# Kernel optimization log

Hardware: AMD Instinct MI355X
Metric: run time of the kernel (lower is better)

Reference implementation:

```python
import jax, jax.numpy as jnp
import numpy as np
import math

VOCAB = 32000
D_MODEL = 1024
CTX = 2048
B, T = 4, 2048
NUM_Q_HEADS = 16
NUM_KV_GROUPS = 4
HEAD_DIM = D_MODEL // NUM_Q_HEADS          # 64
REP = NUM_Q_HEADS // NUM_KV_GROUPS         # queries per KV group = 4
HALF = D_MODEL // 2                        # token/pos embedding width


def setup_inputs() -> dict:
    key = jax.random.key(0)
    ks = jax.random.split(key, 12)
    s = 0.02
    idx = jax.random.randint(ks[0], (B, T), 0, VOCAB, dtype=jnp.int32)
    mask = jnp.tril(jnp.ones((T, T), dtype=jnp.int32))  # causal mask, 0 = blocked
    return {
        "idx": idx,
        "mask": mask,
        "tok_table": jax.random.normal(ks[1], (VOCAB, HALF), jnp.float32) * s,
        "pos_table": jax.random.normal(ks[2], (CTX, HALF), jnp.float32) * s,
        "W_q": jax.random.normal(ks[3], (D_MODEL, D_MODEL), jnp.float32) * s,
        "b_q": jnp.zeros((D_MODEL,), jnp.float32),
        "W_k": jax.random.normal(ks[4], (D_MODEL, NUM_KV_GROUPS * HEAD_DIM), jnp.float32) * s,
        "b_k": jnp.zeros((NUM_KV_GROUPS * HEAD_DIM,), jnp.float32),
        "W_v": jax.random.normal(ks[5], (D_MODEL, NUM_KV_GROUPS * HEAD_DIM), jnp.float32) * s,
        "b_v": jnp.zeros((NUM_KV_GROUPS * HEAD_DIM,), jnp.float32),
        "W_o": jax.random.normal(ks[6], (D_MODEL, D_MODEL), jnp.float32) * s,
        "b_o": jnp.zeros((D_MODEL,), jnp.float32),
    }


def reference(idx, mask, tok_table, pos_table, W_q, b_q, W_k, b_k, W_v, b_v, W_o, b_o):
    Bd, Td = idx.shape
    # token + position embedding, concatenated along feature dim -> [B, T, D_MODEL]
    tok_emb = tok_table[idx]                              # [B, T, HALF]
    pos_emb = pos_table[jnp.arange(Td)]                   # [T, HALF]
    x = jnp.concatenate([tok_emb, jnp.broadcast_to(pos_emb, (Bd, Td, HALF))], axis=-1)

    # GQA projections
    Q = (x @ W_q + b_q).reshape(Bd, Td, NUM_Q_HEADS, HEAD_DIM).transpose(0, 2, 1, 3)   # [B,H,T,D]
    K = (x @ W_k + b_k).reshape(Bd, Td, NUM_KV_GROUPS, HEAD_DIM).transpose(0, 2, 1, 3) # [B,G,T,D]
    V = (x @ W_v + b_v).reshape(Bd, Td, NUM_KV_GROUPS, HEAD_DIM).transpose(0, 2, 1, 3)
    # repeat_interleave KV groups to match query heads (naive GQA expansion)
    K = jnp.repeat(K, REP, axis=1)                        # [B,H,T,D]
    V = jnp.repeat(V, REP, axis=1)

    scale = 1.0 / math.sqrt(HEAD_DIM)
    scores = jnp.einsum('bhqd,bhkd->bhqk', Q, K) * scale  # [B,H,T,T]
    scores = jnp.where(mask == 0, jnp.float32(-1e9), scores)
    probs = jax.nn.softmax(scores, axis=-1)
    attn = jnp.einsum('bhqk,bhkd->bhqd', probs, V)        # [B,H,T,D]
    attn = attn.transpose(0, 2, 1, 3).reshape(Bd, Td, D_MODEL)
    return attn @ W_o + b_o
```

## Files before the change

### kernel.cpp

```cpp
#include <hip/hip_runtime.h>

typedef unsigned short u16;
typedef __attribute__((ext_vector_type(8))) short bf16x8;
typedef __attribute__((ext_vector_type(4))) float f32x4;

__device__ __forceinline__ u16 f2bf(float f) {
  union { float f; unsigned u; } x; x.f = f;
  unsigned r = x.u + 0x7fffu + ((x.u >> 16) & 1u);
  return (u16)(r >> 16);
}
__device__ __forceinline__ float bf2f(u16 u) {
  union { unsigned u; float f; } x; x.u = ((unsigned)u) << 16;
  return x.f;
}

#define GLOAD_LDS16(gp, lp)                                              \
  __builtin_amdgcn_global_load_lds(                                      \
      (const __attribute__((address_space(1))) unsigned int*)(gp),       \
      (__attribute__((address_space(3))) unsigned int*)(lp), 16, 0, 0)

__global__ __launch_bounds__(256) void transpose_w(const float* __restrict__ in,
                                                   u16* __restrict__ out, int N) {
  __shared__ float tile[32][33];
  const int n0 = blockIdx.x * 32, k0 = blockIdx.y * 32;
  const int tx = threadIdx.x & 31, ty = threadIdx.x >> 5;
#pragma unroll
  for (int i = 0; i < 4; ++i) {
    int k = k0 + ty + i * 8;
    tile[ty + i * 8][tx] = in[(size_t)k * N + n0 + tx];
  }
  __syncthreads();
#pragma unroll
  for (int i = 0; i < 4; ++i) {
    int n = n0 + ty + i * 8;
    out[(size_t)n * 1024 + k0 + tx] = f2bf(tile[tx][ty + i * 8]);
  }
}

__global__ __launch_bounds__(256) void embed_kernel(const int* __restrict__ idx,
                                                    const float* __restrict__ tok,
                                                    const float* __restrict__ pos,
                                                    u16* __restrict__ x) {
  const int r = blockIdx.x;
  const int t = r & 2047;
  const int tok_id = idx[r];
  const int c = threadIdx.x * 4;
  float4 v;
  if (c < 512)
    v = *(const float4*)&tok[(size_t)tok_id * 512 + c];
  else
    v = *(const float4*)&pos[(size_t)t * 512 + (c - 512)];
  ushort4 o;
  o.x = f2bf(v.x); o.y = f2bf(v.y); o.z = f2bf(v.z); o.w = f2bf(v.w);
  *(ushort4*)&x[(size_t)r * 1024 + c] = o;
}

__global__ __launch_bounds__(256) void gemm_qkv(const u16* __restrict__ A,
                                                const u16* __restrict__ Bt,
                                                const float* __restrict__ bq,
                                                const float* __restrict__ bk,
                                                const float* __restrict__ bv,
                                                u16* __restrict__ Qb, u16* __restrict__ Kb,
                                                u16* __restrict__ Vb) {
  __shared__ u16 Alds[128 * 32];
  __shared__ u16 Blds[128 * 32];
  const int tid = threadIdx.x;
  const int lane = tid & 63, w = tid >> 6;
  const int ln = lane & 15, lm = lane >> 4;
  const int wm = w & 1, wn = w >> 1;
  const int bm = blockIdx.y, bn = blockIdx.x;
  f32x4 acc[4][4] = {};
  const size_t arow0 = (size_t)bm * 128;
  const size_t brow0 = (size_t)bn * 128;
  for (int ks = 0; ks < 1024; ks += 32) {
    __syncthreads();
#pragma unroll
    for (int it = 0; it < 2; ++it) {
      const int idx = it * 256 + tid;
      const int row = idx >> 2, ko = idx & 3;
      GLOAD_LDS16(A + (arow0 + row) * 1024 + ks + ko * 8, &Alds[idx * 8]);
      GLOAD_LDS16(Bt + (brow0 + row) * 1024 + ks + ko * 8, &Blds[idx * 8]);
    }
    asm volatile("s_waitcnt vmcnt(0)" ::: "memory");
    __syncthreads();
    bf16x8 af[4], bfr[4];
#pragma unroll
    for (int m = 0; m < 4; ++m)
      af[m] = *(const bf16x8*)&Alds[(wm * 64 + m * 16 + ln) * 32 + lm * 8];
#pragma unroll
    for (int n = 0; n < 4; ++n)
      bfr[n] = *(const bf16x8*)&Blds[(wn * 64 + n * 16 + ln) * 32 + lm * 8];
#pragma unroll
    for (int m = 0; m < 4; ++m)
#pragma unroll
      for (int n = 0; n < 4; ++n)
        acc[m][n] = __builtin_amdgcn_mfma_f32_16x16x32_bf16(af[m], bfr[n], acc[m][n], 0, 0, 0);
  }
#pragma unroll
  for (int m = 0; m < 4; ++m) {
    const int rg0 = bm * 128 + wm * 64 + m * 16 + lm * 4;
#pragma unroll
    for (int n = 0; n < 4; ++n) {
      const int cg = bn * 128 + wn * 64 + n * 16 + ln;
      float bias;
      if (cg < 1024) bias = bq[cg];
      else if (cg < 1280) bias = bk[cg - 1024];
      else bias = bv[cg - 1280];
#pragma unroll
      for (int r = 0; r < 4; ++r) {
        const int rr = rg0 + r;
        const int bb = rr >> 11, tt = rr & 2047;
        const float v = acc[m][n][r] + bias;
        if (cg < 1024) {
          Qb[(((size_t)bb * 16 + (cg >> 6)) * 2048 + tt) * 64 + (cg & 63)] = f2bf(v);
        } else if (cg < 1280) {
          const int c2 = cg - 1024;
          Kb[(((size_t)bb * 4 + (c2 >> 6)) * 2048 + tt) * 64 + (c2 & 63)] = f2bf(v);
        } else {
          const int c2 = cg - 1280;
          Vb[(((size_t)bb * 4 + (c2 >> 6)) * 2048 + tt) * 64 + (c2 & 63)] = f2bf(v);
        }
      }
    }
  }
}

__global__ __launch_bounds__(256) void transpose_v(const u16* __restrict__ V,
                                                   u16* __restrict__ Vt) {
  __shared__ u16 tile[32][33];
  const int bg = blockIdx.z;
  const int d0 = blockIdx.x * 32, t0 = blockIdx.y * 32;
  const int tx = threadIdx.x & 31, ty = threadIdx.x >> 5;
  const u16* Vin = V + (size_t)bg * 2048 * 64;
  u16* Vout = Vt + (size_t)bg * 64 * 2048;
#pragma unroll
  for (int i = 0; i < 4; ++i)
    tile[ty + i * 8][tx] = Vin[(size_t)(t0 + ty + i * 8) * 64 + d0 + tx];
  __syncthreads();
#pragma unroll
  for (int i = 0; i < 4; ++i)
    Vout[(size_t)(d0 + ty + i * 8) * 2048 + t0 + tx] = tile[tx][ty + i * 8];
}

__global__ __launch_bounds__(512) void attn_kernel(const u16* __restrict__ Qb,
                                                   const u16* __restrict__ Kb,
                                                   const u16* __restrict__ Vt,
                                                   u16* __restrict__ attn) {
  __shared__ u16 Plds[8][16 * 32];
  const int tid = threadIdx.x;
  const int lane = tid & 63, ww = tid >> 6;
  const int w = ww & 3, half = ww >> 2;
  const int ln = lane & 15, lm = lane >> 4;
  const int pair = blockIdx.x;
  const int bh = blockIdx.y;
  const int b = bh >> 4, h = bh & 15, g = h >> 2;
  const u16* Qp = Qb + (size_t)bh * 2048 * 64;
  const u16* Kp = Kb + (size_t)(b * 4 + g) * 2048 * 64;
  const u16* Vp = Vt + (size_t)(b * 4 + g) * 64 * 2048;

  const int qt = half ? (31 - pair) : pair;
  const int qw0 = qt * 64 + w * 16;

  bf16x8 qf[2];
  {
    const int qrow = qw0 + ln;
#pragma unroll
    for (int c = 0; c < 2; ++c) {
      bf16x8 raw = *(const bf16x8*)(Qp + (size_t)qrow * 64 + c * 32 + lm * 8);
#pragma unroll
      for (int i = 0; i < 8; ++i) raw[i] = (short)f2bf(bf2f((u16)raw[i]) * 0.125f);
      qf[c] = raw;
    }
  }

  f32x4 o[4] = {};
  float l_r[4] = {0.0f, 0.0f, 0.0f, 0.0f};

  const int nfull = qw0 >> 5;
  for (int kb = 0; kb <= nfull; ++kb) {
    const int kv0 = kb * 32;
    f32x4 s[2] = {};
#pragma unroll
    for (int n = 0; n < 2; ++n) {
#pragma unroll
      for (int c = 0; c < 2; ++c) {
        const bf16x8 kf =
            *(const bf16x8*)(Kp + (size_t)(kv0 + n * 16 + ln) * 64 + c * 32 + lm * 8);
        s[n] = __builtin_amdgcn_mfma_f32_16x16x32_bf16(qf[c], kf, s[n], 0, 0, 0);
      }
    }
    bf16x8 vf[4];
#pragma unroll
    for (int nd = 0; nd < 4; ++nd)
      vf[nd] = *(const bf16x8*)(Vp + (size_t)(nd * 16 + ln) * 2048 + kv0 + lm * 8);

    if (kb == nfull) {
#pragma unroll
      for (int n = 0; n < 2; ++n)
#pragma unroll
        for (int r = 0; r < 4; ++r) {
          const int kv = kv0 + n * 16 + ln;
          const int q = qw0 + lm * 4 + r;
          if (kv > q) s[n][r] = -1.0e30f;
        }
    }
#pragma unroll
    for (int n = 0; n < 2; ++n)
#pragma unroll
      for (int r = 0; r < 4; ++r) s[n][r] = __expf(s[n][r]);
#pragma unroll
    for (int r = 0; r < 4; ++r) l_r[r] += s[0][r] + s[1][r];

#pragma unroll
    for (int n = 0; n < 2; ++n)
#pragma unroll
      for (int r = 0; r < 4; ++r) {
        const int row = lm * 4 + r, col = n * 16 + ln;
        const int slot = (col >> 3) ^ ((row >> 1) & 3);
        Plds[ww][row * 32 + slot * 8 + (col & 7)] = f2bf(s[n][r]);
      }
    asm volatile("s_waitcnt lgkmcnt(0)" ::: "memory");
    const bf16x8 pf = *(const bf16x8*)&Plds[ww][ln * 32 + (lm ^ ((ln >> 1) & 3)) * 8];
#pragma unroll
    for (int nd = 0; nd < 4; ++nd)
      o[nd] = __builtin_amdgcn_mfma_f32_16x16x32_bf16(pf, vf[nd], o[nd], 0, 0, 0);
  }
#pragma unroll
  for (int off = 1; off < 16; off <<= 1)
#pragma unroll
    for (int r = 0; r < 4; ++r) l_r[r] += __shfl_xor(l_r[r], off);

  float invl[4];
#pragma unroll
  for (int r = 0; r < 4; ++r) invl[r] = 1.0f / l_r[r];
#pragma unroll
  for (int nd = 0; nd < 4; ++nd)
#pragma unroll
    for (int r = 0; r < 4; ++r) {
      const int q = qw0 + lm * 4 + r;
      const int col = h * 64 + nd * 16 + ln;
      attn[((size_t)b * 2048 + q) * 1024 + col] = f2bf(o[nd][r] * invl[r]);
    }
}

__global__ __launch_bounds__(256) void gemm_out(const u16* __restrict__ A,
                                                const u16* __restrict__ Bt,
                                                const float* __restrict__ bo,
                                                float* __restrict__ out) {
  __shared__ u16 Alds[128 * 32];
  __shared__ u16 Blds[128 * 32];
  const int tid = threadIdx.x;
  const int lane = tid & 63, w = tid >> 6;
  const int ln = lane & 15, lm = lane >> 4;
  const int wm = w & 1, wn = w >> 1;
  const int bm = blockIdx.y, bn = blockIdx.x;
  f32x4 acc[4][4] = {};
  const size_t arow0 = (size_t)bm * 128;
  const size_t brow0 = (size_t)bn * 128;
  for (int ks = 0; ks < 1024; ks += 32) {
    __syncthreads();
#pragma unroll
    for (int it = 0; it < 2; ++it) {
      const int idx = it * 256 + tid;
      const int row = idx >> 2, ko = idx & 3;
      GLOAD_LDS16(A + (arow0 + row) * 1024 + ks + ko * 8, &Alds[idx * 8]);
      GLOAD_LDS16(Bt + (brow0 + row) * 1024 + ks + ko * 8, &Blds[idx * 8]);
    }
    asm volatile("s_waitcnt vmcnt(0)" ::: "memory");
    __syncthreads();
    bf16x8 af[4], bfr[4];
#pragma unroll
    for (int m = 0; m < 4; ++m)
      af[m] = *(const bf16x8*)&Alds[(wm * 64 + m * 16 + ln) * 32 + lm * 8];
#pragma unroll
    for (int n = 0; n < 4; ++n)
      bfr[n] = *(const bf16x8*)&Blds[(wn * 64 + n * 16 + ln) * 32 + lm * 8];
#pragma unroll
    for (int m = 0; m < 4; ++m)
#pragma unroll
      for (int n = 0; n < 4; ++n)
        acc[m][n] = __builtin_amdgcn_mfma_f32_16x16x32_bf16(af[m], bfr[n], acc[m][n], 0, 0, 0);
  }
#pragma unroll
  for (int m = 0; m < 4; ++m) {
    const int rg0 = bm * 128 + wm * 64 + m * 16 + lm * 4;
#pragma unroll
    for (int n = 0; n < 4; ++n) {
      const int cg = bn * 128 + wn * 64 + n * 16 + ln;
      const float bias = bo[cg];
#pragma unroll
      for (int r = 0; r < 4; ++r)
        out[(size_t)(rg0 + r) * 1024 + cg] = acc[m][n][r] + bias;
    }
  }
}

extern "C" void kernel_launch(void* const* d_in, const int* in_sizes, int n_in,
                              void* d_out, int out_size, void* d_ws, size_t ws_size,
                              hipStream_t stream) {
  const int* idx = (const int*)d_in[0];
  const float* tok = (const float*)d_in[2];
  const float* pos = (const float*)d_in[3];
  const float* Wq = (const float*)d_in[4];
  const float* bq = (const float*)d_in[5];
  const float* Wk = (const float*)d_in[6];
  const float* bk = (const float*)d_in[7];
  const float* Wv = (const float*)d_in[8];
  const float* bv = (const float*)d_in[9];
  const float* Wo = (const float*)d_in[10];
  const float* bo = (const float*)d_in[11];
  float* out = (float*)d_out;

  char* ws = (char*)d_ws;
  u16* x_bf   = (u16*)(ws);
  u16* wqkv_t = (u16*)(ws + 16777216);
  u16* wo_t   = (u16*)(ws + 19922944);
  u16* Qb     = (u16*)(ws + 22020096);
  u16* Kb     = (u16*)(ws + 38797312);
  u16* Vb     = (u16*)(ws + 42991616);
  u16* Vt     = (u16*)(ws + 47185920);

  transpose_w<<<dim3(32, 32), 256, 0, stream>>>(Wq, wqkv_t, 1024);
  transpose_w<<<dim3(8, 32), 256, 0, stream>>>(Wk, wqkv_t + (size_t)1024 * 1024, 256);
  transpose_w<<<dim3(8, 32), 256, 0, stream>>>(Wv, wqkv_t + (size_t)1280 * 1024, 256);
  transpose_w<<<dim3(32, 32), 256, 0, stream>>>(Wo, wo_t, 1024);
  embed_kernel<<<8192, 256, 0, stream>>>(idx, tok, pos, x_bf);
  gemm_qkv<<<dim3(12, 64), 256, 0, stream>>>(x_bf, wqkv_t, bq, bk, bv, Qb, Kb, Vb);
  transpose_v<<<dim3(2, 64, 16), 256, 0, stream>>>(Vb, Vt);
  attn_kernel<<<dim3(16, 64), 512, 0, stream>>>(Qb, Kb, Vt, x_bf);
  gemm_out<<<dim3(8, 64), 256, 0, stream>>>(x_bf, wo_t, bo, out);
}
```

Before: 502.1 us.

## Split KV range across wave halves and combine partial attention via LDS

Instead of each half of the block processing a different query tile, both halves now process the same query tile in turn, each covering half of the KV blocks. Partial outputs and row sums from the second half are combined through shared memory before normalisation and the write. Launch bounds also request higher occupancy. The intent is to shorten each wave's serial KV loop and balance work, at the cost of extra syncthreads, LDS traffic and register-pressure limits.

```diff
diff --git a/kernel.cpp b/kernel.cpp
--- a/kernel.cpp
+++ b/kernel.cpp
@@ -142,11 +142,12 @@
     Vout[(size_t)(d0 + ty + i * 8) * 2048 + t0 + tx] = tile[tx][ty + i * 8];
 }
 
-__global__ __launch_bounds__(512) void attn_kernel(const u16* __restrict__ Qb,
-                                                   const u16* __restrict__ Kb,
-                                                   const u16* __restrict__ Vt,
-                                                   u16* __restrict__ attn) {
+__global__ __launch_bounds__(512, 8) void attn_kernel(const u16* __restrict__ Qb,
+                                                      const u16* __restrict__ Kb,
+                                                      const u16* __restrict__ Vt,
+                                                      u16* __restrict__ attn) {
   __shared__ u16 Plds[8][16 * 32];
+  __shared__ float Comb[4][64][20];
   const int tid = threadIdx.x;
   const int lane = tid & 63, ww = tid >> 6;
   const int w = ww & 3, half = ww >> 2;
@@ -158,89 +159,115 @@
   const u16* Kp = Kb + (size_t)(b * 4 + g) * 2048 * 64;
   const u16* Vp = Vt + (size_t)(b * 4 + g) * 64 * 2048;
 
-  const int qt = half ? (31 - pair) : pair;
-  const int qw0 = qt * 64 + w * 16;
-
-  bf16x8 qf[2];
-  {
-    const int qrow = qw0 + ln;
-#pragma unroll
-    for (int c = 0; c < 2; ++c) {
-      bf16x8 raw = *(const bf16x8*)(Qp + (size_t)qrow * 64 + c * 32 + lm * 8);
-#pragma unroll
-      for (int i = 0; i < 8; ++i) raw[i] = (short)f2bf(bf2f((u16)raw[i]) * 0.125f);
-      qf[c] = raw;
-    }
-  }
-
-  f32x4 o[4] = {};
-  float l_r[4] = {0.0f, 0.0f, 0.0f, 0.0f};
-
-  const int nfull = qw0 >> 5;
-  for (int kb = 0; kb <= nfull; ++kb) {
-    const int kv0 = kb * 32;
-    f32x4 s[2] = {};
-#pragma unroll
-    for (int n = 0; n < 2; ++n) {
+#pragma unroll
+  for (int tile = 0; tile < 2; ++tile) {
+    const int qt = tile ? (31 - pair) : pair;
+    const int qw0 = qt * 64 + w * 16;
+
+    bf16x8 qf[2];
+    {
+      const int qrow = qw0 + ln;
 #pragma unroll
       for (int c = 0; c < 2; ++c) {
-        const bf16x8 kf =
-            *(const bf16x8*)(Kp + (size_t)(kv0 + n * 16 + ln) * 64 + c * 32 + lm * 8);
-        s[n] = __builtin_amdgcn_mfma_f32_16x16x32_bf16(qf[c], kf, s[n], 0, 0, 0);
+        bf16x8 raw = *(const bf16x8*)(Qp + (size_t)qrow * 64 + c * 32 + lm * 8);
+#pragma unroll
+        for (int i = 0; i < 8; ++i) raw[i] = (short)f2bf(bf2f((u16)raw[i]) * 0.125f);
+        qf[c] = raw;
       }
     }
-    bf16x8 vf[4];
-#pragma unroll
-    for (int nd = 0; nd < 4; ++nd)
-      vf[nd] = *(const bf16x8*)(Vp + (size_t)(nd * 16 + ln) * 2048 + kv0 + lm * 8);
-
-    if (kb == nfull) {
-#pragma unroll
-      for (int n = 0; n < 2; ++n)
+
+    f32x4 o[4] = {};
+    float l_r[4] = {0.0f, 0.0f, 0.0f, 0.0f};
+
+    const int n = (qw0 >> 5) + 1;
+    const int mid = (n + 1) >> 1;
+    const int kb0 = half ? mid : 0;
+    const int kb1 = half ? n : mid;
+
+    for (int kb = kb0; kb < kb1; ++kb) {
+      const int kv0 = kb * 32;
+      f32x4 s[2] = {};
+#pragma unroll
+      for (int nn = 0; nn < 2; ++nn) {
+#pragma unroll
+        for (int c = 0; c < 2; ++c) {
+          const bf16x8 kf =
+              *(const bf16x8*)(Kp + (size_t)(kv0 + nn * 16 + ln) * 64 + c * 32 + lm * 8);
+          s[nn] = __builtin_amdgcn_mfma_f32_16x16x32_bf16(qf[c], kf, s[nn], 0, 0, 0);
+        }
+      }
+      bf16x8 vf[4];
+#pragma unroll
+      for (int nd = 0; nd < 4; ++nd)
+        vf[nd] = *(const bf16x8*)(Vp + (size_t)(nd * 16 + ln) * 2048 + kv0 + lm * 8);
+
+      if (kb == n - 1) {
+#pragma unroll
+        for (int nn = 0; nn < 2; ++nn)
+#pragma unroll
+          for (int r = 0; r < 4; ++r) {
+            const int kv = kv0 + nn * 16 + ln;
+            const int q = qw0 + lm * 4 + r;
+            if (kv > q) s[nn][r] = -1.0e30f;
+          }
+      }
+#pragma unroll
+      for (int nn = 0; nn < 2; ++nn)
+#pragma unroll
+        for (int r = 0; r < 4; ++r) s[nn][r] = __expf(s[nn][r]);
+#pragma unroll
+      for (int r = 0; r < 4; ++r) l_r[r] += s[0][r] + s[1][r];
+
+#pragma unroll
+      for (int nn = 0; nn < 2; ++nn)
 #pragma unroll
         for (int r = 0; r < 4; ++r) {
-          const int kv = kv0 + n * 16 + ln;
+          const int row = lm * 4 + r, col = nn * 16 + ln;
+          const int slot = (col >> 3) ^ ((row >> 1) & 3);
+          Plds[ww][row * 32 + slot * 8 + (col & 7)] = f2bf(s[nn][r]);
+        }
+      asm volatile("s_waitcnt lgkmcnt(0)" ::: "memory");
+      const bf16x8 pf = *(const bf16x8*)&Plds[ww][ln * 32 + (lm ^ ((ln >> 1) & 3)) * 8];
+#pragma unroll
+      for (int nd = 0; nd < 4; ++nd)
+        o[nd] = __builtin_amdgcn_mfma_f32_16x16x32_bf16(pf, vf[nd], o[nd], 0, 0, 0);
+    }
+#pragma unroll
+    for (int off = 1; off < 16; off <<= 1)
+#pragma unroll
+      for (int r = 0; r < 4; ++r) l_r[r] += __shfl_xor(l_r[r], off);
+
+    if (half) {
+#pragma unroll
+      for (int nd = 0; nd < 4; ++nd)
+#pragma unroll
+        for (int r = 0; r < 4; ++r) Comb[w][lane][nd * 4 + r] = o[nd][r];
+#pragma unroll
+      for (int r = 0; r < 4; ++r) Comb[w][lane][16 + r] = l_r[r];
+    }
+    __syncthreads();
+    if (!half) {
+#pragma unroll
+      for (int nd = 0; nd < 4; ++nd)
+#pragma unroll
+        for (int r = 0; r < 4; ++r) o[nd][r] += Comb[w][lane][nd * 4 + r];
+#pragma unroll
+      for (int r = 0; r < 4; ++r) l_r[r] += Comb[w][lane][16 + r];
+
+      float invl[4];
+#pragma unroll
+      for (int r = 0; r < 4; ++r) invl[r] = 1.0f / l_r[r];
+#pragma unroll
+      for (int nd = 0; nd < 4; ++nd)
+#pragma unroll
+        for (int r = 0; r < 4; ++r) {
           const int q = qw0 + lm * 4 + r;
-          if (kv > q) s[n][r] = -1.0e30f;
+          const int col = h * 64 + nd * 16 + ln;
+          attn[((size_t)b * 2048 + q) * 1024 + col] = f2bf(o[nd][r] * invl[r]);
         }
     }
-#pragma unroll
-    for (int n = 0; n < 2; ++n)
-#pragma unroll
-      for (int r = 0; r < 4; ++r) s[n][r] = __expf(s[n][r]);
-#pragma unroll
-    for (int r = 0; r < 4; ++r) l_r[r] += s[0][r] + s[1][r];
-
-#pragma unroll
-    for (int n = 0; n < 2; ++n)
-#pragma unroll
-      for (int r = 0; r < 4; ++r) {
-        const int row = lm * 4 + r, col = n * 16 + ln;
-        const int slot = (col >> 3) ^ ((row >> 1) & 3);
-        Plds[ww][row * 32 + slot * 8 + (col & 7)] = f2bf(s[n][r]);
-      }
-    asm volatile("s_waitcnt lgkmcnt(0)" ::: "memory");
-    const bf16x8 pf = *(const bf16x8*)&Plds[ww][ln * 32 + (lm ^ ((ln >> 1) & 3)) * 8];
-#pragma unroll
-    for (int nd = 0; nd < 4; ++nd)
-      o[nd] = __builtin_amdgcn_mfma_f32_16x16x32_bf16(pf, vf[nd], o[nd], 0, 0, 0);
-  }
-#pragma unroll
-  for (int off = 1; off < 16; off <<= 1)
-#pragma unroll
-    for (int r = 0; r < 4; ++r) l_r[r] += __shfl_xor(l_r[r], off);
-
-  float invl[4];
-#pragma unroll
-  for (int r = 0; r < 4; ++r) invl[r] = 1.0f / l_r[r];
-#pragma unroll
-  for (int nd = 0; nd < 4; ++nd)
-#pragma unroll
-    for (int r = 0; r < 4; ++r) {
-      const int q = qw0 + lm * 4 + r;
-      const int col = h * 64 + nd * 16 + ln;
-      attn[((size_t)b * 2048 + q) * 1024 + col] = f2bf(o[nd][r] * invl[r]);
-    }
+    __syncthreads();
+  }
 }
 
 __global__ __launch_bounds__(256) void gemm_out(const u16* __restrict__ A,
```

After: 559.3 us. 11.4% more time.
